# Performance work log

Hardware: AMD Instinct MI355X
Metric: run time of the kernel (lower is better)

## Reference

```python
import jax, jax.numpy as jnp
import numpy as np

SEQ, WORD, EMBED, NHEAD = 2048, 1024, 128, 16


def setup_inputs() -> dict:
    key = jax.random.key(0)
    ks = jax.random.split(key, 6)
    sw = 1.0 / np.sqrt(WORD)  # xavier-ish scale for linear weights
    sp = 1.0 / np.sqrt(EMBED * NHEAD)
    return {
        "x": jax.random.normal(ks[0], (SEQ, WORD), jnp.float32),
        "Wq": jax.random.normal(ks[1], (NHEAD, WORD, EMBED), jnp.float32) * sw,
        "bq": jnp.zeros((NHEAD, EMBED), jnp.float32),
        "Wk": jax.random.normal(ks[2], (NHEAD, WORD, EMBED), jnp.float32) * sw,
        "bk": jnp.zeros((NHEAD, EMBED), jnp.float32),
        "Wv": jax.random.normal(ks[3], (NHEAD, WORD, EMBED), jnp.float32) * sw,
        "bv": jnp.zeros((NHEAD, EMBED), jnp.float32),
        "proj": jax.random.normal(ks[4], (NHEAD * EMBED, EMBED), jnp.float32) * sp,
    }


def reference(x, Wq, bq, Wk, bk, Wv, bv, proj):
    # Batched-head equivalent of the per-head Attention ModuleList loop.
    # x: [S, W]; Wq/Wk/Wv: [H, W, E]; b*: [H, E]; proj: [H*E, E]
    Q = jnp.einsum("sw,hwe->hse", x, Wq) + bq[:, None, :]
    K = jnp.einsum("sw,hwe->hse", x, Wk) + bk[:, None, :]
    V = jnp.einsum("sw,hwe->hse", x, Wv) + bv[:, None, :]
    scale = 1.0 / jnp.sqrt(jnp.asarray(EMBED, x.dtype))
    scores = jnp.einsum("hqe,hke->hqk", Q, K) * scale  # [H, S, S]
    attn = jax.nn.softmax(scores, axis=-1)
    Z = jnp.einsum("hqk,hke->hqe", attn, V)  # [H, S, E]
    # torch.cat([...], dim=1): per-head outputs side-by-side -> [S, H*E]
    Z_s = jnp.transpose(Z, (1, 0, 2)).reshape(x.shape[0], -1)
    return Z_s @ proj  # [S, E]
```

## Files before the change

kernel.cpp:

```cpp
#include <hip/hip_runtime.h>
#include <stdint.h>

#define GAS __attribute__((address_space(1)))
#define LAS __attribute__((address_space(3)))

typedef unsigned short u16;
typedef __attribute__((ext_vector_type(8))) __bf16 bf16x8;
typedef __attribute__((ext_vector_type(4))) float f32x4;

#define SEQ 2048
#define WORD 1024
#define EMBED 128
#define NHEAD 16

__device__ __forceinline__ u16 f2b(float f) {
  return __builtin_bit_cast(u16, (__bf16)f);
}

__global__ __launch_bounds__(256) void cast_x_kernel(const float* __restrict__ x,
                                                     u16* __restrict__ xb) {
  int i = (blockIdx.x * 256 + threadIdx.x) * 4;
  float4 v = *(const float4*)(x + i);
  ushort4 o;
  o.x = f2b(v.x); o.y = f2b(v.y); o.z = f2b(v.z); o.w = f2b(v.w);
  *(ushort4*)(xb + i) = o;
}

__global__ __launch_bounds__(256) void transpose_cast_kernel(
    const float* __restrict__ s0, const float* __restrict__ s1,
    const float* __restrict__ s2, u16* __restrict__ d0, u16* __restrict__ d1,
    u16* __restrict__ d2, int R, int C, long stride, int zsel) {
  __shared__ float tile[32][33];
  const float* s;
  u16* d;
  if (zsel) {
    int z = blockIdx.z;
    int wsel = z >> 4, hh = z & 15;
    s = (wsel == 0 ? s0 : wsel == 1 ? s1 : s2) + (long)hh * stride;
    d = (wsel == 0 ? d0 : wsel == 1 ? d1 : d2) + (long)hh * stride;
  } else {
    s = s0; d = d0;
  }
  int r0 = blockIdx.x * 32, c0 = blockIdx.y * 32;
  int tx = threadIdx.x & 31, ty = threadIdx.x >> 5;
#pragma unroll
  for (int i = 0; i < 4; ++i)
    tile[ty + i * 8][tx] = s[(long)(r0 + ty + i * 8) * C + c0 + tx];
  __syncthreads();
#pragma unroll
  for (int i = 0; i < 4; ++i)
    d[(long)(c0 + ty + i * 8) * R + r0 + tx] = f2b(tile[tx][ty + i * 8]);
}

template <typename OUT>
__device__ __forceinline__ void gemm128(const u16* __restrict__ A, const u16* __restrict__ B,
                                        OUT* __restrict__ C, int lda, int ldb, int ldc,
                                        int ksteps, const float* biasN, const float* biasM,
                                        float scale) {
  __shared__ u16 lA[128 * 64];
  __shared__ u16 lB[128 * 64];
  const int tid = threadIdx.x;
  const int l = tid & 63, w = tid >> 6;
  const int quad = l >> 4, ln = l & 15;
  const int wm = w >> 1, wn = w & 1;
  f32x4 acc[4][4] = {};
  for (int ks = 0; ks < ksteps; ++ks) {
    const u16* Ak = A + ks * 64;
    const u16* Bk = B + ks * 64;
    __syncthreads();
#pragma unroll
    for (int i = 0; i < 4; ++i) {
      int idx = w * 256 + i * 64 + l;
      int r = idx >> 3, cp = idx & 7;
      int cg = cp ^ (r & 7);
      __builtin_amdgcn_global_load_lds((const GAS void*)(Ak + (long)r * lda + cg * 8),
                                       (LAS void*)(lA + (w * 256 + i * 64) * 8), 16, 0, 0);
      __builtin_amdgcn_global_load_lds((const GAS void*)(Bk + (long)r * ldb + cg * 8),
                                       (LAS void*)(lB + (w * 256 + i * 64) * 8), 16, 0, 0);
    }
    __syncthreads();
    bf16x8 af[2][4], bfv[2][4];
#pragma unroll
    for (int kc = 0; kc < 2; ++kc) {
#pragma unroll
      for (int i = 0; i < 4; ++i) {
        int c = kc * 4 + quad;
        int rm = wm * 64 + i * 16 + ln;
        af[kc][i] = *(const bf16x8*)(lA + rm * 64 + ((c ^ (rm & 7)) * 8));
        int rn = wn * 64 + i * 16 + ln;
        bfv[kc][i] = *(const bf16x8*)(lB + rn * 64 + ((c ^ (rn & 7)) * 8));
      }
    }
#pragma unroll
    for (int kc = 0; kc < 2; ++kc)
#pragma unroll
      for (int i = 0; i < 4; ++i)
#pragma unroll
        for (int j = 0; j < 4; ++j)
          acc[i][j] = __builtin_amdgcn_mfma_f32_16x16x32_bf16(af[kc][i], bfv[kc][j],
                                                              acc[i][j], 0, 0, 0);
  }
#pragma unroll
  for (int i = 0; i < 4; ++i) {
#pragma unroll
    for (int j = 0; j < 4; ++j) {
      int row0 = wm * 64 + i * 16 + quad * 4;
      int col = wn * 64 + j * 16 + ln;
      float bn = biasN ? biasN[col] : 0.f;
#pragma unroll
      for (int reg = 0; reg < 4; ++reg) {
        int row = row0 + reg;
        float bm = biasM ? biasM[row] : 0.f;
        float v = (acc[i][j][reg] + bn + bm) * scale;
        if constexpr (sizeof(OUT) == 2)
          C[(long)row * ldc + col] = (OUT)f2b(v);
        else
          C[(long)row * ldc + col] = v;
      }
    }
  }
}

__global__ __launch_bounds__(256, 3) void qkv_gemm_kernel(
    const u16* __restrict__ xb, const u16* __restrict__ Wqt, const u16* __restrict__ Wkt,
    const u16* __restrict__ Wvt, const float* __restrict__ bq, const float* __restrict__ bk,
    const float* __restrict__ bv, u16* __restrict__ Q, u16* __restrict__ Kb,
    u16* __restrict__ Vt) {
  const int t = blockIdx.x;
  const int h = blockIdx.y;
  const int which = blockIdx.z;
  const float qscale = 0.12753042123789493f;
  if (which == 0) {
    gemm128<u16>(xb + t * 128 * WORD, Wqt + h * EMBED * WORD,
                 Q + h * SEQ * EMBED + t * 128 * EMBED, WORD, WORD, EMBED,
                 WORD / 64, bq + h * EMBED, nullptr, qscale);
  } else if (which == 1) {
    gemm128<u16>(xb + t * 128 * WORD, Wkt + h * EMBED * WORD,
                 Kb + h * SEQ * EMBED + t * 128 * EMBED, WORD, WORD, EMBED,
                 WORD / 64, bk + h * EMBED, nullptr, 1.f);
  } else {
    gemm128<u16>(Wvt + h * EMBED * WORD, xb + t * 128 * WORD,
                 Vt + h * EMBED * SEQ + t * 128, WORD, WORD, SEQ,
                 WORD / 64, nullptr, bv + h * EMBED, 1.f);
  }
}

__global__ __launch_bounds__(256, 2) void attn_kernel(const u16* __restrict__ Q,
                                                      const u16* __restrict__ K,
                                                      const u16* __restrict__ V,
                                                      u16* __restrict__ Zs) {
  __shared__ u16 lKV[4 * 8192];
  __shared__ u16 lP[4 * 16 * 72];
  const int h = blockIdx.y, qb = blockIdx.x;
  const int tid = threadIdx.x;
  const int l = tid & 63, w = tid >> 6, quad = l >> 4, ln = l & 15;
  const int wr = w >> 1, wk = w & 1;
  const u16* Qh = Q + h * SEQ * EMBED;
  const u16* Kh = K + h * SEQ * EMBED;
  const u16* Vh = V + h * EMBED * SEQ;
  u16* Pw = lP + w * (16 * 72);
  const int q0 = qb * 64 + wr * 32;
  const u16* myK = lKV + wk * 8192;
  const u16* myV = lKV + 16384 + wk * 8192;

  bf16x8 qf[2][4];
#pragma unroll
  for (int rs = 0; rs < 2; ++rs)
#pragma unroll
    for (int kc = 0; kc < 4; ++kc)
      qf[rs][kc] = *(const bf16x8*)(Qh + (q0 + rs * 16 + ln) * EMBED + kc * 32 + quad * 8);

  const __bf16 ov = (ln == 0) ? (__bf16)1.0f : (__bf16)0.0f;
  const bf16x8 onesf = {ov, ov, ov, ov, ov, ov, ov, ov};

  f32x4 oacc[2][8] = {};
  f32x4 lacc[2] = {};

  for (int sup = 0; sup < SEQ / 128; ++sup) {
    __syncthreads();
#pragma unroll
    for (int j = 0; j < 8; ++j) {
      int kb = j >> 2;
      int cb = (j & 3) * 256 + w * 64;
      int c = cb + l;
      int rk = c >> 4, cgk = (c & 15) ^ (rk & 15);
      __builtin_amdgcn_global_load_lds(
          (const GAS void*)(Kh + (sup * 128 + kb * 64 + rk) * EMBED + cgk * 8),
          (LAS void*)(lKV + kb * 8192 + cb * 8), 16, 0, 0);
      int rv = c >> 3, cgv = (c & 7) ^ (rv & 7);
      __builtin_amdgcn_global_load_lds(
          (const GAS void*)(Vh + rv * SEQ + sup * 128 + kb * 64 + cgv * 8),
          (LAS void*)(lKV + 16384 + kb * 8192 + cb * 8), 16, 0, 0);
    }
    __syncthreads();
    f32x4 sacc[2][4] = {};
#pragma unroll
    for (int kc = 0; kc < 4; ++kc) {
      bf16x8 kf[4];
#pragma unroll
      for (int ns = 0; ns < 4; ++ns) {
        int kr = ns * 16 + ln;
        kf[ns] = *(const bf16x8*)(myK + kr * 128 + (((kc * 4 + quad) ^ (kr & 15)) * 8));
      }
#pragma unroll
      for (int ns = 0; ns < 4; ++ns)
#pragma unroll
        for (int rs = 0; rs < 2; ++rs)
          sacc[rs][ns] = __builtin_amdgcn_mfma_f32_16x16x32_bf16(qf[rs][kc], kf[ns],
                                                                 sacc[rs][ns], 0, 0, 0);
    }
    bf16x8 vf[2][8];
#pragma unroll
    for (int kc = 0; kc < 2; ++kc)
#pragma unroll
      for (int es = 0; es < 8; ++es) {
        int er = es * 16 + ln;
        vf[kc][es] = *(const bf16x8*)(myV + er * 64 + (((kc * 4 + quad) ^ (er & 7)) * 8));
      }
#pragma unroll
    for (int rs = 0; rs < 2; ++rs) {
#pragma unroll
      for (int ns = 0; ns < 4; ++ns)
#pragma unroll
        for (int r = 0; r < 4; ++r)
          Pw[(quad * 4 + r) * 72 + ns * 16 + ln] = f2b(exp2f(sacc[rs][ns][r]));
#pragma unroll
      for (int kc = 0; kc < 2; ++kc) {
        bf16x8 pa = *(const bf16x8*)(Pw + ln * 72 + kc * 32 + quad * 8);
#pragma unroll
        for (int es = 0; es < 8; ++es)
          oacc[rs][es] = __builtin_amdgcn_mfma_f32_16x16x32_bf16(pa, vf[kc][es],
                                                                 oacc[rs][es], 0, 0, 0);
        lacc[rs] = __builtin_amdgcn_mfma_f32_16x16x32_bf16(pa, onesf, lacc[rs], 0, 0, 0);
      }
    }
  }
  __syncthreads();
  float* lO = (float*)lKV;
  if (wk == 1) {
#pragma unroll
    for (int rs = 0; rs < 2; ++rs) {
#pragma unroll
      for (int es = 0; es < 8; ++es)
#pragma unroll
        for (int r = 0; r < 4; ++r)
          lO[wr * 4224 + (rs * 16 + quad * 4 + r) * 132 + es * 16 + ln] = oacc[rs][es][r];
      if (ln == 0)
#pragma unroll
        for (int r = 0; r < 4; ++r)
          lO[wr * 4224 + (rs * 16 + quad * 4 + r) * 132 + 128] = lacc[rs][r];
    }
  }
  __syncthreads();
  if (wk == 0) {
#pragma unroll
    for (int rs = 0; rs < 2; ++rs)
#pragma unroll
      for (int r = 0; r < 4; ++r) {
        int lrow = rs * 16 + quad * 4 + r;
        float lsum = __shfl(lacc[rs][r], l & 48) + lO[wr * 4224 + lrow * 132 + 128];
        float rl = 1.f / lsum;
        int srow = q0 + lrow;
#pragma unroll
        for (int es = 0; es < 8; ++es) {
          float o = oacc[rs][es][r] + lO[wr * 4224 + lrow * 132 + es * 16 + ln];
          Zs[(long)srow * (NHEAD * EMBED) + h * EMBED + es * 16 + ln] = f2b(o * rl);
        }
      }
  }
}

__global__ __launch_bounds__(256, 2) void final_gemm_kernel(const u16* __restrict__ Zs,
                                                            const u16* __restrict__ projT,
                                                            float* __restrict__ pbuf) {
  const int t = blockIdx.x;
  const int kc = blockIdx.y;
  gemm128<float>(Zs + (long)t * 128 * (NHEAD * EMBED) + kc * 256, projT + kc * 256,
                 pbuf + (long)kc * SEQ * EMBED + t * 128 * EMBED,
                 NHEAD * EMBED, NHEAD * EMBED, EMBED, 4, nullptr, nullptr, 1.f);
}

__global__ __launch_bounds__(256) void reduce_kernel(const float* __restrict__ pbuf,
                                                     float* __restrict__ out) {
  int i = (blockIdx.x * 256 + threadIdx.x) * 4;
  float4 s = {0.f, 0.f, 0.f, 0.f};
#pragma unroll
  for (int kc = 0; kc < 8; ++kc) {
    float4 v = *(const float4*)(pbuf + (long)kc * SEQ * EMBED + i);
    s.x += v.x; s.y += v.y; s.z += v.z; s.w += v.w;
  }
  *(float4*)(out + i) = s;
}

extern "C" void kernel_launch(void* const* d_in, const int* in_sizes, int n_in,
                              void* d_out, int out_size, void* d_ws, size_t ws_size,
                              hipStream_t stream) {
  const float* x    = (const float*)d_in[0];
  const float* Wq   = (const float*)d_in[1];
  const float* bq   = (const float*)d_in[2];
  const float* Wk   = (const float*)d_in[3];
  const float* bk   = (const float*)d_in[4];
  const float* Wv   = (const float*)d_in[5];
  const float* bv   = (const float*)d_in[6];
  const float* proj = (const float*)d_in[7];
  float* out = (float*)d_out;

  char* ws = (char*)d_ws;
  u16* xb    = (u16*)(ws);
  u16* Wqt   = (u16*)(ws + (4L << 20));
  u16* Wkt   = (u16*)(ws + (8L << 20));
  u16* Wvt   = (u16*)(ws + (12L << 20));
  u16* projT = (u16*)(ws + (16L << 20));
  u16* Qm    = (u16*)(ws + (17L << 20));
  u16* Km    = (u16*)(ws + (26L << 20));
  u16* Vt    = (u16*)(ws + (35L << 20));
  u16* Zs    = (u16*)(ws + (44L << 20));
  float* pbuf = (float*)(ws);

  cast_x_kernel<<<dim3(SEQ * WORD / 1024), dim3(256), 0, stream>>>(x, xb);
  transpose_cast_kernel<<<dim3(WORD / 32, EMBED / 32, 48), dim3(256), 0, stream>>>(
      Wq, Wk, Wv, Wqt, Wkt, Wvt, WORD, EMBED, (long)WORD * EMBED, 1);
  transpose_cast_kernel<<<dim3(SEQ / 32, EMBED / 32, 1), dim3(256), 0, stream>>>(
      proj, nullptr, nullptr, projT, nullptr, nullptr, SEQ, EMBED, 0, 0);

  qkv_gemm_kernel<<<dim3(16, NHEAD, 3), dim3(256), 0, stream>>>(
      xb, Wqt, Wkt, Wvt, bq, bk, bv, Qm, Km, Vt);

  attn_kernel<<<dim3(32, NHEAD), dim3(256), 0, stream>>>(Qm, Km, Vt, Zs);

  final_gemm_kernel<<<dim3(16, 8), dim3(256), 0, stream>>>(Zs, projT, pbuf);
  reduce_kernel<<<dim3(SEQ * EMBED / 1024), dim3(256), 0, stream>>>(pbuf, out);
}
```

Before: 200.0 us.

## Prefetch next K/V tile into registers during compute and raise MFMA priority

The first K/V tile is now loaded into LDS before the main loop. Each iteration then issues global loads of the next tile into registers, runs the QK and PV MFMAs on the current tile, and writes the staged registers to LDS after a barrier. This aims to hide global-memory latency behind matrix math instead of stalling on direct global-to-LDS loads at the top of each iteration. s_setprio is also raised around the MFMA groups to favour this wave's issue. The 16 extra float4 staging registers add VGPR pressure, which may lower occupancy or cause spills.

```diff
diff --git a/kernel.cpp b/kernel.cpp
--- a/kernel.cpp
+++ b/kernel.cpp
@@ -173,26 +173,39 @@
   const __bf16 ov = (ln == 0) ? (__bf16)1.0f : (__bf16)0.0f;
   const bf16x8 onesf = {ov, ov, ov, ov, ov, ov, ov, ov};
 
+#pragma unroll
+  for (int j = 0; j < 8; ++j) {
+    int kb = j >> 2;
+    int cb = (j & 3) * 256 + w * 64;
+    int c = cb + l;
+    int rk = c >> 4, cgk = (c & 15) ^ (rk & 15);
+    __builtin_amdgcn_global_load_lds(
+        (const GAS void*)(Kh + (kb * 64 + rk) * EMBED + cgk * 8),
+        (LAS void*)(lKV + kb * 8192 + cb * 8), 16, 0, 0);
+    int rv = c >> 3, cgv = (c & 7) ^ (rv & 7);
+    __builtin_amdgcn_global_load_lds(
+        (const GAS void*)(Vh + rv * SEQ + kb * 64 + cgv * 8),
+        (LAS void*)(lKV + 16384 + kb * 8192 + cb * 8), 16, 0, 0);
+  }
+
   f32x4 oacc[2][8] = {};
   f32x4 lacc[2] = {};
 
   for (int sup = 0; sup < SEQ / 128; ++sup) {
     __syncthreads();
-#pragma unroll
-    for (int j = 0; j < 8; ++j) {
-      int kb = j >> 2;
-      int cb = (j & 3) * 256 + w * 64;
-      int c = cb + l;
-      int rk = c >> 4, cgk = (c & 15) ^ (rk & 15);
-      __builtin_amdgcn_global_load_lds(
-          (const GAS void*)(Kh + (sup * 128 + kb * 64 + rk) * EMBED + cgk * 8),
-          (LAS void*)(lKV + kb * 8192 + cb * 8), 16, 0, 0);
-      int rv = c >> 3, cgv = (c & 7) ^ (rv & 7);
-      __builtin_amdgcn_global_load_lds(
-          (const GAS void*)(Vh + rv * SEQ + sup * 128 + kb * 64 + cgv * 8),
-          (LAS void*)(lKV + 16384 + kb * 8192 + cb * 8), 16, 0, 0);
-    }
-    __syncthreads();
+    float4 stK[8], stV[8];
+    const int pf = (sup + 1 < SEQ / 128);
+    if (pf) {
+#pragma unroll
+      for (int j = 0; j < 8; ++j) {
+        int kb = j >> 2;
+        int c = (j & 3) * 256 + w * 64 + l;
+        int rk = c >> 4, cgk = (c & 15) ^ (rk & 15);
+        stK[j] = *(const float4*)(Kh + ((sup + 1) * 128 + kb * 64 + rk) * EMBED + cgk * 8);
+        int rv = c >> 3, cgv = (c & 7) ^ (rv & 7);
+        stV[j] = *(const float4*)(Vh + rv * SEQ + (sup + 1) * 128 + kb * 64 + cgv * 8);
+      }
+    }
     f32x4 sacc[2][4] = {};
 #pragma unroll
     for (int kc = 0; kc < 4; ++kc) {
@@ -202,12 +215,14 @@
         int kr = ns * 16 + ln;
         kf[ns] = *(const bf16x8*)(myK + kr * 128 + (((kc * 4 + quad) ^ (kr & 15)) * 8));
       }
+      __builtin_amdgcn_s_setprio(1);
 #pragma unroll
       for (int ns = 0; ns < 4; ++ns)
 #pragma unroll
         for (int rs = 0; rs < 2; ++rs)
           sacc[rs][ns] = __builtin_amdgcn_mfma_f32_16x16x32_bf16(qf[rs][kc], kf[ns],
                                                                  sacc[rs][ns], 0, 0, 0);
+      __builtin_amdgcn_s_setprio(0);
     }
     bf16x8 vf[2][8];
 #pragma unroll
@@ -227,11 +242,23 @@
 #pragma unroll
       for (int kc = 0; kc < 2; ++kc) {
         bf16x8 pa = *(const bf16x8*)(Pw + ln * 72 + kc * 32 + quad * 8);
+        __builtin_amdgcn_s_setprio(1);
 #pragma unroll
         for (int es = 0; es < 8; ++es)
           oacc[rs][es] = __builtin_amdgcn_mfma_f32_16x16x32_bf16(pa, vf[kc][es],
                                                                  oacc[rs][es], 0, 0, 0);
         lacc[rs] = __builtin_amdgcn_mfma_f32_16x16x32_bf16(pa, onesf, lacc[rs], 0, 0, 0);
+        __builtin_amdgcn_s_setprio(0);
+      }
+    }
+    __syncthreads();
+    if (pf) {
+#pragma unroll
+      for (int j = 0; j < 8; ++j) {
+        int kb = j >> 2;
+        int c = (j & 3) * 256 + w * 64 + l;
+        *(float4*)(lKV + kb * 8192 + c * 8) = stK[j];
+        *(float4*)(lKV + 16384 + kb * 8192 + c * 8) = stV[j];
       }
     }
   }
```

Result: slower. 304.1 us (+52.1%).

## Double-buffer K/V tiles in attention with larger 8-wave blocks and MFMA priority

Applied to the files above, without the earlier changes.

The attention kernel now runs 512-thread blocks covering 128 query rows each. It keeps two LDS buffers for the K/V tiles and issues the async global-to-LDS loads for the next tile while the current one is being computed, using explicit vmcnt waits and raw barriers. It also raises wave priority around the MFMA bursts and remaps block IDs so each group of blocks shares heads. The goal is to hide K/V load latency and cut sync stalls. The cost is that LDS use roughly doubles, which caps occupancy at one block per CU.

```diff
diff --git a/kernel.cpp b/kernel.cpp
--- a/kernel.cpp
+++ b/kernel.cpp
@@ -145,13 +145,15 @@
   }
 }
 
-__global__ __launch_bounds__(256, 2) void attn_kernel(const u16* __restrict__ Q,
+__global__ __launch_bounds__(512, 2) void attn_kernel(const u16* __restrict__ Q,
                                                       const u16* __restrict__ K,
                                                       const u16* __restrict__ V,
                                                       u16* __restrict__ Zs) {
-  __shared__ u16 lKV[4 * 8192];
-  __shared__ u16 lP[4 * 16 * 72];
-  const int h = blockIdx.y, qb = blockIdx.x;
+  __shared__ u16 lKV[2][4 * 8192];
+  __shared__ u16 lP[8 * 16 * 72];
+  const int bid = blockIdx.x;
+  const int swz = (bid & 7) * 32 + (bid >> 3);
+  const int h = swz >> 4, qb = swz & 15;
   const int tid = threadIdx.x;
   const int l = tid & 63, w = tid >> 6, quad = l >> 4, ln = l & 15;
   const int wr = w >> 1, wk = w & 1;
@@ -159,40 +161,58 @@
   const u16* Kh = K + h * SEQ * EMBED;
   const u16* Vh = V + h * EMBED * SEQ;
   u16* Pw = lP + w * (16 * 72);
-  const int q0 = qb * 64 + wr * 32;
-  const u16* myK = lKV + wk * 8192;
-  const u16* myV = lKV + 16384 + wk * 8192;
-
-  bf16x8 qf[2][4];
-#pragma unroll
-  for (int rs = 0; rs < 2; ++rs)
-#pragma unroll
-    for (int kc = 0; kc < 4; ++kc)
-      qf[rs][kc] = *(const bf16x8*)(Qh + (q0 + rs * 16 + ln) * EMBED + kc * 32 + quad * 8);
-
-  const __bf16 ov = (ln == 0) ? (__bf16)1.0f : (__bf16)0.0f;
-  const bf16x8 onesf = {ov, ov, ov, ov, ov, ov, ov, ov};
-
-  f32x4 oacc[2][8] = {};
-  f32x4 lacc[2] = {};
-
-  for (int sup = 0; sup < SEQ / 128; ++sup) {
-    __syncthreads();
-#pragma unroll
-    for (int j = 0; j < 8; ++j) {
-      int kb = j >> 2;
-      int cb = (j & 3) * 256 + w * 64;
+  const int q0 = qb * 128 + wr * 32;
+
+  auto stage = [&](int buf, int sup) {
+#pragma unroll
+    for (int j = 0; j < 4; ++j) {
+      int kb = j >> 1;
+      int cb = (j & 1) * 512 + w * 64;
       int c = cb + l;
       int rk = c >> 4, cgk = (c & 15) ^ (rk & 15);
       __builtin_amdgcn_global_load_lds(
           (const GAS void*)(Kh + (sup * 128 + kb * 64 + rk) * EMBED + cgk * 8),
-          (LAS void*)(lKV + kb * 8192 + cb * 8), 16, 0, 0);
+          (LAS void*)(&lKV[buf][kb * 8192 + cb * 8]), 16, 0, 0);
       int rv = c >> 3, cgv = (c & 7) ^ (rv & 7);
       __builtin_amdgcn_global_load_lds(
           (const GAS void*)(Vh + rv * SEQ + sup * 128 + kb * 64 + cgv * 8),
-          (LAS void*)(lKV + 16384 + kb * 8192 + cb * 8), 16, 0, 0);
-    }
-    __syncthreads();
+          (LAS void*)(&lKV[buf][16384 + kb * 8192 + cb * 8]), 16, 0, 0);
+    }
+  };
+
+  bf16x8 qf[2][4];
+#pragma unroll
+  for (int rs = 0; rs < 2; ++rs)
+#pragma unroll
+    for (int kc = 0; kc < 4; ++kc)
+      qf[rs][kc] = *(const bf16x8*)(Qh + (q0 + rs * 16 + ln) * EMBED + kc * 32 + quad * 8);
+
+  const __bf16 ov = (ln == 0) ? (__bf16)1.0f : (__bf16)0.0f;
+  const bf16x8 onesf = {ov, ov, ov, ov, ov, ov, ov, ov};
+
+  f32x4 oacc[2][8] = {};
+  f32x4 lacc[2] = {};
+
+  stage(0, 0);
+  asm volatile("s_waitcnt vmcnt(0)" ::: "memory");
+  __builtin_amdgcn_s_barrier();
+  __builtin_amdgcn_sched_barrier(0);
+
+  int cur = 0;
+#pragma unroll 1
+  for (int sup = 0; sup < SEQ / 128; ++sup) {
+    if (sup + 1 < SEQ / 128) {
+      stage(cur ^ 1, sup + 1);
+      asm volatile("s_waitcnt vmcnt(8)" ::: "memory");
+    } else {
+      asm volatile("s_waitcnt vmcnt(0)" ::: "memory");
+    }
+    __builtin_amdgcn_s_barrier();
+    __builtin_amdgcn_sched_barrier(0);
+
+    const u16* myK = &lKV[cur][wk * 8192];
+    const u16* myV = &lKV[cur][16384 + wk * 8192];
+
     f32x4 sacc[2][4] = {};
 #pragma unroll
     for (int kc = 0; kc < 4; ++kc) {
@@ -202,12 +222,14 @@
         int kr = ns * 16 + ln;
         kf[ns] = *(const bf16x8*)(myK + kr * 128 + (((kc * 4 + quad) ^ (kr & 15)) * 8));
       }
+      __builtin_amdgcn_s_setprio(1);
 #pragma unroll
       for (int ns = 0; ns < 4; ++ns)
 #pragma unroll
         for (int rs = 0; rs < 2; ++rs)
           sacc[rs][ns] = __builtin_amdgcn_mfma_f32_16x16x32_bf16(qf[rs][kc], kf[ns],
                                                                  sacc[rs][ns], 0, 0, 0);
+      __builtin_amdgcn_s_setprio(0);
     }
     bf16x8 vf[2][8];
 #pragma unroll
@@ -227,13 +249,18 @@
 #pragma unroll
       for (int kc = 0; kc < 2; ++kc) {
         bf16x8 pa = *(const bf16x8*)(Pw + ln * 72 + kc * 32 + quad * 8);
+        __builtin_amdgcn_s_setprio(1);
 #pragma unroll
         for (int es = 0; es < 8; ++es)
           oacc[rs][es] = __builtin_amdgcn_mfma_f32_16x16x32_bf16(pa, vf[kc][es],
                                                                  oacc[rs][es], 0, 0, 0);
         lacc[rs] = __builtin_amdgcn_mfma_f32_16x16x32_bf16(pa, onesf, lacc[rs], 0, 0, 0);
-      }
-    }
+        __builtin_amdgcn_s_setprio(0);
+      }
+    }
+    __builtin_amdgcn_sched_barrier(0);
+    __builtin_amdgcn_s_barrier();
+    cur ^= 1;
   }
   __syncthreads();
   float* lO = (float*)lKV;
@@ -326,7 +353,7 @@
   qkv_gemm_kernel<<<dim3(16, NHEAD, 3), dim3(256), 0, stream>>>(
       xb, Wqt, Wkt, Wvt, bq, bk, bv, Qm, Km, Vt);
 
-  attn_kernel<<<dim3(32, NHEAD), dim3(256), 0, stream>>>(Qm, Km, Vt, Zs);
+  attn_kernel<<<dim3(256), dim3(512), 0, stream>>>(Qm, Km, Vt, Zs);
 
   final_gemm_kernel<<<dim3(16, 8), dim3(256), 0, stream>>>(Zs, projT, pbuf);
   reduce_kernel<<<dim3(SEQ * EMBED / 1024), dim3(256), 0, stream>>>(pbuf, out);
```

After: 194.9 us. -2.5%, faster.
